# Performance work log

Measured on AMD Instinct MI355X. Metric: run time of the kernel, lower is better.

## Reference

```python
import jax, jax.numpy as jnp
import numpy as np

T, B, I, H, L = 1024, 16, 1024, 1024, 2


def setup_inputs() -> dict:
    key = jax.random.key(0)
    ks = jax.random.split(key, 1 + 4 * L)
    k = 1.0 / np.sqrt(H)
    inp = {"x": jax.random.normal(ks[0], (T, B, I), dtype=jnp.float32)}
    for l in range(L):
        base = 1 + 4 * l
        in_dim = I if l == 0 else H
        inp[f"Wih_{l}"] = jax.random.uniform(ks[base + 0], (4 * H, in_dim), minval=-k, maxval=k, dtype=jnp.float32)
        inp[f"bih_{l}"] = jax.random.uniform(ks[base + 1], (4 * H,), minval=-k, maxval=k, dtype=jnp.float32)
        inp[f"Whh_{l}"] = jax.random.uniform(ks[base + 2], (4 * H, H), minval=-k, maxval=k, dtype=jnp.float32)
        inp[f"bhh_{l}"] = jax.random.uniform(ks[base + 3], (4 * H,), minval=-k, maxval=k, dtype=jnp.float32)
    return inp


def _lstm_layer(x, Wih, bih, Whh, bhh):
    # x: [T, B, in_dim] time-major. Returns (outputs [T,B,H], h_T [B,H], c_T [B,H]).
    Hd = Whh.shape[1]
    Bn = x.shape[1]
    h0 = jnp.zeros((Bn, Hd), dtype=x.dtype)
    c0 = jnp.zeros((Bn, Hd), dtype=x.dtype)
    # Precompute input projection for all timesteps in one big GEMM.
    gx = jnp.einsum('tbi,gi->tbg', x, Wih) + bih  # [T, B, 4H]

    def step(carry, gxt):
        h, c = carry
        gates = gxt + h @ Whh.T + bhh  # [B, 4H]
        i, f, g, o = jnp.split(gates, 4, axis=1)
        i = jax.nn.sigmoid(i)
        f = jax.nn.sigmoid(f)
        g = jnp.tanh(g)
        o = jax.nn.sigmoid(o)
        c = f * c + i * g
        h = o * jnp.tanh(c)
        return (h, c), h

    (hT, cT), ys = jax.lax.scan(step, (h0, c0), gx)
    return ys, hT, cT


def reference(x, Wih_0, bih_0, Whh_0, bhh_0, Wih_1, bih_1, Whh_1, bhh_1):
    out0, h0, c0 = _lstm_layer(x, Wih_0, bih_0, Whh_0, bhh_0)
    out1, h1, c1 = _lstm_layer(out0, Wih_1, bih_1, Whh_1, bhh_1)
    next_h = jnp.stack([h0, h1])  # [num_layers, B, H]
    next_c = jnp.stack([c0, c1])
    return out1, (next_h, next_c)
```

## Files before the change

kernel.cpp:

```cpp
#include <hip/hip_runtime.h>


#define T_STEPS 1024
#define TQ 16

typedef unsigned short u16;
typedef unsigned long long u64;
typedef __attribute__((ext_vector_type(8))) __bf16 bf16x8;
typedef __attribute__((ext_vector_type(4))) float float4v;
typedef __attribute__((ext_vector_type(4))) unsigned short ushort4v;
typedef __attribute__((ext_vector_type(8))) unsigned short ushort8;

__device__ __forceinline__ float bf2f(u16 h) {
    unsigned u = ((unsigned)h) << 16;
    return __builtin_bit_cast(float, u);
}
__device__ __forceinline__ u16 f2bf(float f) {
    unsigned u = __builtin_bit_cast(unsigned, f);
    u += 0x7fff + ((u >> 16) & 1);
    return (u16)(u >> 16);
}

__device__ __forceinline__ float4v mfma16(bf16x8 a, bf16x8 b, float4v c) {
    return __builtin_amdgcn_mfma_f32_16x16x32_bf16(a, b, c, 0, 0, 0);
}
__device__ __forceinline__ unsigned aload(const unsigned* p) {
    return __hip_atomic_load(p, __ATOMIC_RELAXED, __HIP_MEMORY_SCOPE_AGENT);
}
__device__ __forceinline__ void astore(unsigned* p, unsigned v) {
    __hip_atomic_store(p, v, __ATOMIC_RELAXED, __HIP_MEMORY_SCOPE_AGENT);
}
__device__ __forceinline__ void pin(bf16x8& v) {
    asm volatile("" : "+v"(v));
}
__device__ __forceinline__ void gld_lds16c(const void* g, void* l) {
    __builtin_amdgcn_global_load_lds(
        (const __attribute__((address_space(1))) unsigned*)g,
        (__attribute__((address_space(3))) unsigned*)l, 16, 0, 0);
}
__device__ __forceinline__ void gld_lds16b(const void* g, void* l) {
    __builtin_amdgcn_global_load_lds(
        (const __attribute__((address_space(1))) unsigned*)g,
        (__attribute__((address_space(3))) unsigned*)l, 16, 0, 17);
}

__global__ void init_zero(unsigned* __restrict__ flags0,
                          unsigned* __restrict__ flags1,
                          unsigned* __restrict__ h0,
                          unsigned* __restrict__ h1) {
    int i = blockIdx.x * 256 + threadIdx.x;
    const int N0 = 65600, N1 = 256, N2 = 8192, N3 = 8192;
    for (int k = i; k < N0 + N1 + N2 + N3; k += 64 * 256) {
        if (k < N0) flags0[k] = 0u;
        else if (k < N0 + N1) flags1[k - N0] = 0u;
        else if (k < N0 + N1 + N2) h0[k - N0 - N1] = 0u;
        else h1[k - N0 - N1 - N2] = 0u;
    }
}

__device__ __forceinline__ void pack_one(const float* src, u16* dst, int tile, int rowbase) {
    int tid = threadIdx.x;
    ushort8* d = (ushort8*)dst;
#pragma unroll
    for (int it = 0; it < 8; ++it) {
        int c = tid + it * 256;
        int kc = c >> 6, lane = c & 63;
        const float4v* s4 = (const float4v*)(src + (((long)(rowbase + (lane & 15))) << 10)
                                                 + (kc << 5) + ((lane >> 4) << 3));
        float4v lo = s4[0], hi = s4[1];
        ushort8 o;
        o[0] = f2bf(lo[0]); o[1] = f2bf(lo[1]); o[2] = f2bf(lo[2]); o[3] = f2bf(lo[3]);
        o[4] = f2bf(hi[0]); o[5] = f2bf(hi[1]); o[6] = f2bf(hi[2]); o[7] = f2bf(hi[3]);
        d[tile * 2048 + c] = o;
    }
}

__global__ void pack_x(const float* __restrict__ src, u16* __restrict__ dst) {
    pack_one(src, dst, blockIdx.x, blockIdx.x << 4);
}

__global__ void pack_w(const float* __restrict__ w0, const float* __restrict__ w1,
                       const float* __restrict__ w2, const float* __restrict__ w3,
                       u16* __restrict__ d0, u16* __restrict__ d1,
                       u16* __restrict__ d2, u16* __restrict__ d3) {
    int which = blockIdx.x >> 8, tile = blockIdx.x & 255;
    const float* s = (which == 0) ? w0 : (which == 1) ? w1 : (which == 2) ? w2 : w3;
    u16* d = (which == 0) ? d0 : (which == 1) ? d1 : (which == 2) ? d2 : d3;
    int rowbase = ((tile & 3) << 10) + ((tile >> 2) << 4);
    pack_one(s, d, tile, rowbase);
}

__global__ __launch_bounds__(256, 1) void gx_gemm(
        const u16* __restrict__ xp, const bf16x8* __restrict__ wp,
        const float* __restrict__ bih, const float* __restrict__ bhh,
        u16* __restrict__ gx) {
    __shared__ u64 abuf[4096];
    __shared__ float4v part[4][4][64];
    int blk = blockIdx.x, tq = blockIdx.y;
    int tid = threadIdx.x, w = tid >> 6, L = tid & 63;
    int gc = (w << 10) + (blk << 4) + (L & 15);
    float bsum = bih[gc] + bhh[gc];

    bf16x8 wf[32];
#pragma unroll
    for (int g = 0; g < 4; ++g) {
        const bf16x8* wpt = wp + (blk * 4 + g) * 2048 + (w * 8) * 64 + L;
#pragma unroll
        for (int k = 0; k < 8; ++k) wf[g * 8 + k] = wpt[k * 64];
    }
#pragma unroll
    for (int i = 0; i < 32; ++i) pin(wf[i]);
    const bf16x8* hp = (const bf16x8*)abuf;

    const int tch = T_STEPS / TQ;
    for (int tt = 0; tt < tch; ++tt) {
        int t = tq * tch + tt;
        const char* src = (const char*)xp + ((size_t)t << 15) + (w << 13) + (L << 4);
        char* dst = (char*)abuf + (w << 13);
#pragma unroll
        for (int i = 0; i < 8; ++i) gld_lds16c(src + i * 1024, dst + i * 1024);
        __builtin_amdgcn_s_waitcnt(0);
        __builtin_amdgcn_sched_barrier(0);

        float4v acc[4];
#pragma unroll
        for (int g = 0; g < 4; ++g) acc[g] = float4v{0.f, 0.f, 0.f, 0.f};
#pragma unroll
        for (int k = 0; k < 8; ++k) {
            bf16x8 a = hp[(8 * w + k) * 64 + L];
#pragma unroll
            for (int g = 0; g < 4; ++g) acc[g] = mfma16(a, wf[g * 8 + k], acc[g]);
        }
#pragma unroll
        for (int g = 0; g < 4; ++g) part[w][g][L] = acc[g];
        __syncthreads();
        float4v s = part[0][w][L] + part[1][w][L] + part[2][w][L] + part[3][w][L];
        ushort4v o;
#pragma unroll
        for (int r = 0; r < 4; ++r) o[r] = f2bf(s[r] + bsum);
        ((ushort4v*)gx)[((t * 64 + blk) * 4 + w) * 64 + L] = o;
        __syncthreads();
    }
}

__global__ __launch_bounds__(512, 1) void lstm_scan2(
        const u16* __restrict__ gx0,
        const bf16x8* __restrict__ wpHh0,
        const bf16x8* __restrict__ wpIh1, const bf16x8* __restrict__ wpHh1,
        const float* __restrict__ bih1, const float* __restrict__ bhh1,
        unsigned* hist0w,
        unsigned* hist1x,
        unsigned* h1s0,
        unsigned* flags0,
        unsigned* flags1,
        float* outbase) {
    __shared__ u64 hbuf[8192];
    __shared__ float4v lds_part[8][4][64];
    __shared__ float4v lds_g[4][64];

    int tid = threadIdx.x, w = tid >> 6, L = tid & 63;
    int m = tid >> 4, j = tid & 15;
    int Lc = ((m >> 2) << 4) | j, rr = m & 3;
    int layer = (blockIdx.x >= 64);
    int blk = blockIdx.x & 63;
    int hcol = (blk << 4) + j;
    int kcw = hcol >> 5, laneg = (hcol >> 3) & 3, jj = hcol & 7;
    int hwoff32 = ((kcw * 64 + m + (laneg << 4)) << 2) + (jj >> 1);
    float* fH = outbase + 16777216 + (layer ? 16384 : 0);
    float* fC = outbase + 16777216 + 32768 + (layer ? 16384 : 0);
    float c = 0.f;
    const bf16x8* hp = (const bf16x8*)hbuf;

    if (!layer) {
        bf16x8 wf[16];
#pragma unroll
        for (int g = 0; g < 4; ++g) {
            const bf16x8* wsrc = wpHh0 + (blk * 4 + g) * 2048 + (4 * w) * 64 + L;
#pragma unroll
            for (int k = 0; k < 4; ++k) wf[g * 4 + k] = wsrc[k * 64];
        }
#pragma unroll
        for (int i = 0; i < 16; ++i) pin(wf[i]);

        for (int t = 0; t < T_STEPS; ++t) {
            ushort4v gxv = {0, 0, 0, 0};
            if (w < 4) gxv = ((const ushort4v*)gx0)[((t * 64 + blk) * 4 + w) * 64 + L];
            if (t > 0) {
                unsigned v;
                do { v = aload(&flags0[t * 64 + L]); }
                while (__ballot(v != 0u) != ~0ull);
            }
            {
                const char* src = (const char*)hist0w + ((size_t)t << 15) + (w << 12) + (L << 4);
                char* dst = (char*)hbuf + (w << 12);
#pragma unroll
                for (int i = 0; i < 4; ++i) gld_lds16b(src + i * 1024, dst + i * 1024);
            }
            __builtin_amdgcn_s_waitcnt(0);
            __builtin_amdgcn_sched_barrier(0);

            float4v acc[4];
#pragma unroll
            for (int g = 0; g < 4; ++g) acc[g] = float4v{0.f, 0.f, 0.f, 0.f};
#pragma unroll
            for (int k = 0; k < 4; ++k) {
                bf16x8 a = hp[(4 * w + k) * 64 + L];
#pragma unroll
                for (int g = 0; g < 4; ++g) acc[g] = mfma16(a, wf[g * 4 + k], acc[g]);
            }
#pragma unroll
            for (int g = 0; g < 4; ++g) lds_part[w][g][L] = acc[g];
            __syncthreads();

            if (w < 4) {
                float4v s = lds_part[0][w][L] + lds_part[1][w][L]
                          + lds_part[2][w][L] + lds_part[3][w][L]
                          + lds_part[4][w][L] + lds_part[5][w][L]
                          + lds_part[6][w][L] + lds_part[7][w][L];
                float4v g4;
#pragma unroll
                for (int r = 0; r < 4; ++r) g4[r] = s[r] + bf2f(gxv[r]);
                lds_g[w][L] = g4;
            }
            __syncthreads();

            if (tid < 256) {
                float gi = lds_g[0][Lc][rr], gf = lds_g[1][Lc][rr];
                float gg = lds_g[2][Lc][rr], go = lds_g[3][Lc][rr];
                float iv = 1.f / (1.f + __expf(-gi));
                float fv = 1.f / (1.f + __expf(-gf));
                float gv = 1.f - 2.f / (1.f + __expf(2.f * gg));
                float ov = 1.f / (1.f + __expf(-go));
                c = fv * c + iv * gv;
                float h = ov * (1.f - 2.f / (1.f + __expf(2.f * c)));
                unsigned hb = f2bf(h);
                unsigned other = (unsigned)__shfl_xor((int)hb, 1);
                if (!(tid & 1))
                    astore(hist0w + ((size_t)(t + 1) << 13) + hwoff32, hb | (other << 16));
                if (t == T_STEPS - 1) {
                    fH[(m << 10) + hcol] = h;
                    fC[(m << 10) + hcol] = c;
                }
            }
            __builtin_amdgcn_s_waitcnt(0);
            __syncthreads();
            if (tid == 0) astore(&flags0[(t + 1) * 64 + blk], 1u);
        }
    } else {
        bf16x8 wf[32];
#pragma unroll
        for (int g = 0; g < 4; ++g) {
            const bf16x8* wsrc = (w < 4)
                ? (wpIh1 + (blk * 4 + g) * 2048 + (8 * w) * 64 + L)
                : (wpHh1 + (blk * 4 + g) * 2048 + (8 * (w - 4)) * 64 + L);
#pragma unroll
            for (int k = 0; k < 8; ++k) wf[g * 8 + k] = wsrc[k * 64];
        }
#pragma unroll
        for (int i = 0; i < 32; ++i) pin(wf[i]);
        int gc = (w << 10) + (blk << 4) + (L & 15);
        float bsum = (w < 4) ? (bih1[gc] + bhh1[gc]) : 0.f;

        for (int t = 0; t < T_STEPS; ++t) {
            if (w < 4) {
                unsigned v;
                do { v = aload(&flags0[(t + 1) * 64 + L]); }
                while (__ballot(v != 0u) != ~0ull);
            } else if (t > 0) {
                unsigned v;
                do { v = aload(&flags1[(t & 3) * 64 + L]); }
                while (__ballot(v == (unsigned)t) != ~0ull);
            }
            {
                const char* src = (w < 4)
                    ? ((const char*)hist0w + ((size_t)(t + 1) << 15) + (w << 13) + (L << 4))
                    : ((t == 0)
                        ? ((const char*)h1s0 + ((w - 4) << 13) + (L << 4))
                        : ((const char*)hist1x + ((size_t)(t - 1) << 15) + ((w - 4) << 13) + (L << 4)));
                char* dst = (char*)hbuf + (w << 13);
#pragma unroll
                for (int i = 0; i < 8; ++i) gld_lds16b(src + i * 1024, dst + i * 1024);
            }
            __builtin_amdgcn_s_waitcnt(0);
            __builtin_amdgcn_sched_barrier(0);

            float4v acc[4];
#pragma unroll
            for (int g = 0; g < 4; ++g) acc[g] = float4v{0.f, 0.f, 0.f, 0.f};
#pragma unroll
            for (int k = 0; k < 8; ++k) {
                bf16x8 a = hp[(8 * w + k) * 64 + L];
#pragma unroll
                for (int g = 0; g < 4; ++g) acc[g] = mfma16(a, wf[g * 8 + k], acc[g]);
            }
#pragma unroll
            for (int g = 0; g < 4; ++g) lds_part[w][g][L] = acc[g];
            __syncthreads();

            if (w < 4) {
                float4v s = lds_part[0][w][L] + lds_part[1][w][L]
                          + lds_part[2][w][L] + lds_part[3][w][L]
                          + lds_part[4][w][L] + lds_part[5][w][L]
                          + lds_part[6][w][L] + lds_part[7][w][L];
                float4v g4;
#pragma unroll
                for (int r = 0; r < 4; ++r) g4[r] = s[r] + bsum;
                lds_g[w][L] = g4;
            }
            __syncthreads();

            float h = 0.f;
            if (tid < 256) {
                float gi = lds_g[0][Lc][rr], gf = lds_g[1][Lc][rr];
                float gg = lds_g[2][Lc][rr], go = lds_g[3][Lc][rr];
                float iv = 1.f / (1.f + __expf(-gi));
                float fv = 1.f / (1.f + __expf(-gf));
                float gv = 1.f - 2.f / (1.f + __expf(2.f * gg));
                float ov = 1.f / (1.f + __expf(-go));
                c = fv * c + iv * gv;
                h = ov * (1.f - 2.f / (1.f + __expf(2.f * c)));
                unsigned hb = f2bf(h);
                unsigned other = (unsigned)__shfl_xor((int)hb, 1);
                if (!(tid & 1))
                    astore(hist1x + ((size_t)t << 13) + hwoff32, hb | (other << 16));
            }
            __builtin_amdgcn_s_waitcnt(0);
            __syncthreads();
            if (tid == 0) astore(&flags1[(((t + 1) & 3) << 6) + blk], (unsigned)(t + 1));
            if (tid < 256) {
                outbase[(t << 14) + (m << 10) + hcol] = h;
                if (t == T_STEPS - 1) {
                    fH[(m << 10) + hcol] = h;
                    fC[(m << 10) + hcol] = c;
                }
            }
        }
    }
}

extern "C" void kernel_launch(void* const* d_in, const int* in_sizes, int n_in,
                              void* d_out, int out_size, void* d_ws, size_t ws_size,
                              hipStream_t stream) {
    const float* x    = (const float*)d_in[0];
    const float* Wih0 = (const float*)d_in[1];
    const float* bih0 = (const float*)d_in[2];
    const float* Whh0 = (const float*)d_in[3];
    const float* bhh0 = (const float*)d_in[4];
    const float* Wih1 = (const float*)d_in[5];
    const float* bih1 = (const float*)d_in[6];
    const float* Whh1 = (const float*)d_in[7];
    const float* bhh1 = (const float*)d_in[8];
    float* out = (float*)d_out;

    char* ws = (char*)d_ws;
    u16* wpIh0 = (u16*)(ws + 0);
    u16* wpHh0 = (u16*)(ws + 8388608);
    u16* wpIh1 = (u16*)(ws + 16777216);
    u16* wpHh1 = (u16*)(ws + 25165824);
    u16* xpack = (u16*)(ws + 33554432);
    u16* hist0 = (u16*)(ws + 67108864);
    u16* h1s0  = (u16*)(ws + 100696064);
    u16* gxbuf = (u16*)(ws + 100728832);
    unsigned* flags0 = (unsigned*)(ws + 234946560);
    unsigned* flags1 = (unsigned*)(ws + 235208960);

    init_zero<<<dim3(64), dim3(256), 0, stream>>>(flags0, flags1,
                                                  (unsigned*)hist0, (unsigned*)h1s0);
    pack_w<<<dim3(1024), dim3(256), 0, stream>>>(Wih0, Whh0, Wih1, Whh1,
                                                 wpIh0, wpHh0, wpIh1, wpHh1);
    pack_x<<<dim3(1024), dim3(256), 0, stream>>>(x, xpack);
    gx_gemm<<<dim3(64, TQ), dim3(256), 0, stream>>>(
        xpack, (const bf16x8*)wpIh0, bih0, bhh0, gxbuf);
    lstm_scan2<<<dim3(128), dim3(512), 0, stream>>>(
        gxbuf, (const bf16x8*)wpHh0, (const bf16x8*)wpIh1, (const bf16x8*)wpHh1,
        bih1, bhh1, (unsigned*)hist0, (unsigned*)xpack, (unsigned*)h1s0,
        flags0, flags1, out);
}
```

Baseline: 4.814 ms.

## Split layer-1 LSTM scan across 128 blocks with 8 hidden columns each

Layer 1 of the persistent scan kernel is spread over 128 workgroups instead of 64, each owning 8 hidden columns instead of 16. Each workgroup now holds half as many weight fragments and issues half as many MFMAs per step, which should shorten the per-step critical path of the second layer. The flag array grows to 128 entries per slot and every consumer polls two flags per lane. That adds synchronisation traffic, and 192 resident workgroups are needed for the spin-wait scheme to stay deadlock-free.

```diff
diff --git a/kernel.cpp b/kernel.cpp
--- a/kernel.cpp
+++ b/kernel.cpp
@@ -49,7 +49,7 @@
                           unsigned* __restrict__ h0,
                           unsigned* __restrict__ h1) {
     int i = blockIdx.x * 256 + threadIdx.x;
-    const int N0 = 65600, N1 = 256, N2 = 8192, N3 = 8192;
+    const int N0 = 65600, N1 = 512, N2 = 8192, N3 = 8192;
     for (int k = i; k < N0 + N1 + N2 + N3; k += 64 * 256) {
         if (k < N0) flags0[k] = 0u;
         else if (k < N0 + N1) flags1[k - N0] = 0u;
@@ -159,19 +159,20 @@
     __shared__ float4v lds_g[4][64];
 
     int tid = threadIdx.x, w = tid >> 6, L = tid & 63;
-    int m = tid >> 4, j = tid & 15;
-    int Lc = ((m >> 2) << 4) | j, rr = m & 3;
     int layer = (blockIdx.x >= 64);
-    int blk = blockIdx.x & 63;
-    int hcol = (blk << 4) + j;
-    int kcw = hcol >> 5, laneg = (hcol >> 3) & 3, jj = hcol & 7;
-    int hwoff32 = ((kcw * 64 + m + (laneg << 4)) << 2) + (jj >> 1);
-    float* fH = outbase + 16777216 + (layer ? 16384 : 0);
-    float* fC = outbase + 16777216 + 32768 + (layer ? 16384 : 0);
     float c = 0.f;
     const bf16x8* hp = (const bf16x8*)hbuf;
 
     if (!layer) {
+        int blk = blockIdx.x;
+        int m = tid >> 4, j = tid & 15;
+        int Lc = ((m >> 2) << 4) | j, rr = m & 3;
+        int hcol = (blk << 4) + j;
+        int kcw = hcol >> 5, laneg = (hcol >> 3) & 3, jj = hcol & 7;
+        int hwoff32 = ((kcw * 64 + m + (laneg << 4)) << 2) + (jj >> 1);
+        float* fH = outbase + 16777216;
+        float* fC = outbase + 16777216 + 32768;
+
         bf16x8 wf[16];
 #pragma unroll
         for (int g = 0; g < 4; ++g) {
@@ -247,19 +248,37 @@
             if (tid == 0) astore(&flags0[(t + 1) * 64 + blk], 1u);
         }
     } else {
-        bf16x8 wf[32];
-#pragma unroll
-        for (int g = 0; g < 4; ++g) {
-            const bf16x8* wsrc = (w < 4)
-                ? (wpIh1 + (blk * 4 + g) * 2048 + (8 * w) * 64 + L)
-                : (wpHh1 + (blk * 4 + g) * 2048 + (8 * (w - 4)) * 64 + L);
-#pragma unroll
-            for (int k = 0; k < 8; ++k) wf[g * 8 + k] = wsrc[k * 64];
-        }
-#pragma unroll
-        for (int i = 0; i < 32; ++i) pin(wf[i]);
-        int gc = (w << 10) + (blk << 4) + (L & 15);
-        float bsum = (w < 4) ? (bih1[gc] + bhh1[gc]) : 0.f;
+        int blk1 = blockIdx.x - 64;
+        int col8 = L & 7, hi8 = (L >> 3) & 1;
+        int srcl = (L & 48) | (((blk1 & 1) << 3) + col8);
+        int kcb = (w < 4) ? (8 * w) : (8 * (w - 4));
+        const bf16x8* wbase = (w < 4) ? wpIh1 : wpHh1;
+
+        bf16x8 wf[16];
+#pragma unroll
+        for (int p = 0; p < 2; ++p) {
+            int g = 2 * p + hi8;
+            const bf16x8* wsrc = wbase + ((size_t)((blk1 >> 1) * 4 + g)) * 2048
+                                       + kcb * 64 + srcl;
+#pragma unroll
+            for (int k = 0; k < 8; ++k) wf[p * 8 + k] = wsrc[k * 64];
+        }
+#pragma unroll
+        for (int i = 0; i < 16; ++i) pin(wf[i]);
+
+        float bsum = 0.f;
+        if (w < 2) {
+            int g = 2 * w + hi8;
+            int grow = (g << 10) + (blk1 << 3) + col8;
+            bsum = bih1[grow] + bhh1[grow];
+        }
+
+        int m = tid >> 3, j = tid & 7;
+        int hcol = (blk1 << 3) + j;
+        int kcw = hcol >> 5, laneg = (hcol >> 3) & 3, jj = hcol & 7;
+        int hwoff32 = ((kcw * 64 + m + (laneg << 4)) << 2) + (jj >> 1);
+        float* fH = outbase + 16777216 + 16384;
+        float* fC = outbase + 16777216 + 32768 + 16384;
 
         for (int t = 0; t < T_STEPS; ++t) {
             if (w < 4) {
@@ -267,9 +286,11 @@
                 do { v = aload(&flags0[(t + 1) * 64 + L]); }
                 while (__ballot(v != 0u) != ~0ull);
             } else if (t > 0) {
-                unsigned v;
-                do { v = aload(&flags1[(t & 3) * 64 + L]); }
-                while (__ballot(v == (unsigned)t) != ~0ull);
+                unsigned va, vb;
+                do {
+                    va = aload(&flags1[((t & 3) << 7) + L]);
+                    vb = aload(&flags1[((t & 3) << 7) + 64 + L]);
+                } while (__ballot(va == (unsigned)t && vb == (unsigned)t) != ~0ull);
             }
             {
                 const char* src = (w < 4)
@@ -284,20 +305,18 @@
             __builtin_amdgcn_s_waitcnt(0);
             __builtin_amdgcn_sched_barrier(0);
 
-            float4v acc[4];
-#pragma unroll
-            for (int g = 0; g < 4; ++g) acc[g] = float4v{0.f, 0.f, 0.f, 0.f};
+            float4v acc0 = {0.f, 0.f, 0.f, 0.f}, acc1 = {0.f, 0.f, 0.f, 0.f};
 #pragma unroll
             for (int k = 0; k < 8; ++k) {
                 bf16x8 a = hp[(8 * w + k) * 64 + L];
-#pragma unroll
-                for (int g = 0; g < 4; ++g) acc[g] = mfma16(a, wf[g * 8 + k], acc[g]);
-            }
-#pragma unroll
-            for (int g = 0; g < 4; ++g) lds_part[w][g][L] = acc[g];
-            __syncthreads();
-
-            if (w < 4) {
+                acc0 = mfma16(a, wf[k], acc0);
+                acc1 = mfma16(a, wf[8 + k], acc1);
+            }
+            lds_part[w][0][L] = acc0;
+            lds_part[w][1][L] = acc1;
+            __syncthreads();
+
+            if (w < 2) {
                 float4v s = lds_part[0][w][L] + lds_part[1][w][L]
                           + lds_part[2][w][L] + lds_part[3][w][L]
                           + lds_part[4][w][L] + lds_part[5][w][L]
@@ -310,9 +329,12 @@
             __syncthreads();
 
             float h = 0.f;
-            if (tid < 256) {
-                float gi = lds_g[0][Lc][rr], gf = lds_g[1][Lc][rr];
-                float gg = lds_g[2][Lc][rr], go = lds_g[3][Lc][rr];
+            if (tid < 128) {
+                int base = ((m >> 2) << 4), r = m & 3;
+                float gi = lds_g[0][base | j][r];
+                float gf = lds_g[0][base | (8 + j)][r];
+                float gg = lds_g[1][base | j][r];
+                float go = lds_g[1][base | (8 + j)][r];
                 float iv = 1.f / (1.f + __expf(-gi));
                 float fv = 1.f / (1.f + __expf(-gf));
                 float gv = 1.f - 2.f / (1.f + __expf(2.f * gg));
@@ -326,8 +348,8 @@
             }
             __builtin_amdgcn_s_waitcnt(0);
             __syncthreads();
-            if (tid == 0) astore(&flags1[(((t + 1) & 3) << 6) + blk], (unsigned)(t + 1));
-            if (tid < 256) {
+            if (tid == 0) astore(&flags1[(((t + 1) & 3) << 7) + blk1], (unsigned)(t + 1));
+            if (tid < 128) {
                 outbase[(t << 14) + (m << 10) + hcol] = h;
                 if (t == T_STEPS - 1) {
                     fH[(m << 10) + hcol] = h;
@@ -371,7 +393,7 @@
     pack_x<<<dim3(1024), dim3(256), 0, stream>>>(x, xpack);
     gx_gemm<<<dim3(64, TQ), dim3(256), 0, stream>>>(
         xpack, (const bf16x8*)wpIh0, bih0, bhh0, gxbuf);
-    lstm_scan2<<<dim3(128), dim3(512), 0, stream>>>(
+    lstm_scan2<<<dim3(192), dim3(512), 0, stream>>>(
         gxbuf, (const bf16x8*)wpHh0, (const bf16x8*)wpIh1, (const bf16x8*)wpHh1,
         bih1, bhh1, (unsigned*)hist0, (unsigned*)xpack, (unsigned*)h1s0,
         flags0, flags1, out);
```

Result: slower. 5.716 ms (+18.7%).
